# Optimization experiments

Hardware: AMD Instinct MI355X
Metric: run time of the kernel (lower is better)

## Reference

```python
import jax, jax.numpy as jnp
import numpy as np

N = 50000        # nodes
E = 800000       # directed edges (before self-loops)
F_IN = 128       # input node features
HID = 32         # hidden channels per head
HEADS = 4
NCLS = 8
EPS_BN = 1e-5
NEG_SLOPE = 0.2  # GATConv LeakyReLU default


def setup_inputs() -> dict:
    key = jax.random.key(0)
    ks = jax.random.split(key, 16)
    rn = lambda k, shape, s=0.1: jax.random.normal(k, shape, jnp.float32) * s
    inp = {}
    inp["x"] = jax.random.normal(ks[0], (N, F_IN), jnp.float32)
    inp["edge_index"] = jax.random.randint(ks[1], (2, E), 0, N, dtype=jnp.int32)
    # layer 0: F_IN -> HEADS*HID (concat)
    inp["W0"] = rn(ks[2], (F_IN, HEADS * HID))
    inp["as0"] = rn(ks[3], (HEADS, HID))
    inp["ad0"] = rn(ks[4], (HEADS, HID))
    inp["b0"] = jnp.zeros((HEADS * HID,), jnp.float32)
    inp["g0"] = jnp.ones((HEADS * HID,), jnp.float32)
    inp["bb0"] = jnp.zeros((HEADS * HID,), jnp.float32)
    inp["rm0"] = jnp.zeros((HEADS * HID,), jnp.float32)
    inp["rv0"] = jnp.ones((HEADS * HID,), jnp.float32)
    # layer 1: HEADS*HID -> HEADS*HID (concat)
    inp["W1"] = rn(ks[5], (HEADS * HID, HEADS * HID))
    inp["as1"] = rn(ks[6], (HEADS, HID))
    inp["ad1"] = rn(ks[7], (HEADS, HID))
    inp["b1"] = jnp.zeros((HEADS * HID,), jnp.float32)
    inp["g1"] = jnp.ones((HEADS * HID,), jnp.float32)
    inp["bb1"] = jnp.zeros((HEADS * HID,), jnp.float32)
    inp["rm1"] = jnp.zeros((HEADS * HID,), jnp.float32)
    inp["rv1"] = jnp.ones((HEADS * HID,), jnp.float32)
    # layer 2: HEADS*HID -> NCLS, heads=1, concat=False
    inp["W2"] = rn(ks[8], (HEADS * HID, NCLS))
    inp["as2"] = rn(ks[9], (1, NCLS))
    inp["ad2"] = rn(ks[10], (1, NCLS))
    inp["b2"] = jnp.zeros((NCLS,), jnp.float32)
    return inp


def gat_conv(x, src, dst, W, att_s, att_d, bias, H, C, concat):
    """PyG-style GATConv (eval mode, self-loops already appended to src/dst)."""
    n = x.shape[0]
    h = (x @ W).reshape(n, H, C)                       # [N,H,C]
    a_s = (h * att_s).sum(-1)                          # [N,H]
    a_d = (h * att_d).sum(-1)                          # [N,H]
    e = jax.nn.leaky_relu(a_s[src] + a_d[dst], NEG_SLOPE)  # [E,H]
    # numerically-stable segment softmax over incoming edges of each dst node
    m = jax.ops.segment_max(e, dst, num_segments=n)
    m = jnp.where(jnp.isfinite(m), m, 0.0)
    ex = jnp.exp(e - m[dst])
    den = jax.ops.segment_sum(ex, dst, num_segments=n)
    alpha = ex / (den[dst] + 1e-16)                    # [E,H]
    out = jax.ops.segment_sum(h[src] * alpha[:, :, None], dst, num_segments=n)  # [N,H,C]
    out = out.reshape(n, H * C) if concat else out.mean(axis=1)
    return out + bias


def bn_eval(x, g, b, rm, rv):
    return (x - rm) * jax.lax.rsqrt(rv + EPS_BN) * g + b


def reference(x, edge_index, W0, as0, ad0, b0, g0, bb0, rm0, rv0,
              W1, as1, ad1, b1, g1, bb1, rm1, rv1, W2, as2, ad2, b2):
    n = x.shape[0]
    loop = jnp.arange(n, dtype=edge_index.dtype)       # self-loops (PyG default)
    src = jnp.concatenate([edge_index[0], loop])
    dst = jnp.concatenate([edge_index[1], loop])
    h = gat_conv(x, src, dst, W0, as0, ad0, b0, HEADS, HID, True)
    h = jax.nn.elu(bn_eval(h, g0, bb0, rm0, rv0))
    h = gat_conv(h, src, dst, W1, as1, ad1, b1, HEADS, HID, True)
    h = jax.nn.elu(bn_eval(h, g1, bb1, rm1, rv1))
    h = gat_conv(h, src, dst, W2, as2, ad2, b2, 1, NCLS, False)
    return jax.nn.log_softmax(h, axis=1)
```

## Files before the change

kernel.cpp:

```cpp
#include <hip/hip_runtime.h>
#include <hip/hip_cooperative_groups.h>
#include <math.h>

namespace cg = cooperative_groups;

#define N_NODES 50000
#define N_EDGES 800000
#define ET (N_EDGES + N_NODES)
#define NEG 0.2f
#define EPS_BN 1e-5f

#define BSH 8
#define NBUCK ((N_NODES + 255) >> BSH)
#define EPB 4096
#define PB ((ET + EPB - 1) / EPB)
#define CAST_B 3125
#define PACK_B 64
#define GB ((N_NODES + 63) / 64)
#define AGG_U 12500
#define G2B ((N_NODES + 255) / 256)
#define PREP_U (PB + CAST_B + 2 * PACK_B)

typedef __attribute__((ext_vector_type(8))) short short8;
typedef __attribute__((ext_vector_type(4))) float f32x4;

__device__ __forceinline__ float lrelu(float e) { return e > 0.f ? e : NEG * e; }
__device__ __forceinline__ float bflo(unsigned u) { return __uint_as_float(u << 16); }
__device__ __forceinline__ float bfhi(unsigned u) { return __uint_as_float(u & 0xffff0000u); }
__device__ __forceinline__ unsigned f2bf(float f) {
    unsigned b = __float_as_uint(f);
    return (b + 0x7fffu + ((b >> 16) & 1u)) >> 16;
}

struct GatParams {
    const int* ei;
    const float* x;
    const float *W0, *as0, *ad0, *b0, *g0, *bb0, *rm0, *rv0;
    const float *W1, *as1, *ad1, *b1, *g1, *bb1, *rm1, *rv1;
    const float *W2, *as2, *ad2, *b2;
    float* out;
    unsigned short *xb, *Hb, *Xb, *W0p, *W1p;
    int *offs, *boffs, *bcur, *ssrc, *hists;
    int2* pairs;
    float *asn, *adn, *h2;
};


__device__ __forceinline__ void prep_unit(char* smem, int u, int tid,
        const int* __restrict__ ei, int* __restrict__ hists,
        const float* __restrict__ x, unsigned short* __restrict__ xb,
        const float* __restrict__ W0, unsigned short* __restrict__ W0p,
        const float* __restrict__ W1, unsigned short* __restrict__ W1p) {
    if (u < PB) {
        unsigned* h = (unsigned*)smem;
        __syncthreads();
        for (int i = tid; i < NBUCK; i += 256) h[i] = 0;
        __syncthreads();
        int e0 = u * EPB;
        #pragma unroll
        for (int k = 0; k < EPB / 256; k++) {
            int e = e0 + k * 256 + tid;
            if (e < ET) {
                int d = (e < N_EDGES) ? ei[N_EDGES + e] : (e - N_EDGES);
                atomicAdd(&h[d >> BSH], 1u);
            }
        }
        __syncthreads();
        for (int i = tid; i < NBUCK; i += 256)
            hists[u * NBUCK + i] = (int)h[i];
    } else if (u < PB + CAST_B) {
        int i = (u - PB) * 256 + tid;
        const float4* px = (const float4*)x + (size_t)i * 2;
        float4 a = px[0], c = px[1];
        uint4 o;
        o.x = f2bf(a.x) | (f2bf(a.y) << 16);
        o.y = f2bf(a.z) | (f2bf(a.w) << 16);
        o.z = f2bf(c.x) | (f2bf(c.y) << 16);
        o.w = f2bf(c.z) | (f2bf(c.w) << 16);
        ((uint4*)xb)[i] = o;
    } else {
        int pb = u - PB - CAST_B;
        const float* W = (pb < PACK_B) ? W0 : W1;
        unsigned short* Wp = (pb < PACK_B) ? W0p : W1p;
        int o = (pb & (PACK_B - 1)) * 256 + tid;
        int j = o & 7, lane = (o >> 3) & 63, kc = (o >> 9) & 3, t = o >> 11;
        int k = kc * 32 + ((lane >> 4) << 3) + j;
        int n = t * 16 + (lane & 15);
        Wp[o] = (unsigned short)f2bf(W[k * 128 + n]);
    }
}

__device__ __forceinline__ void scan_unit(char* smem, int tid,
        const int* __restrict__ hists, int* __restrict__ boffs,
        int* __restrict__ bcur, int* __restrict__ offs) {
    int* s = (int*)smem;
    int v = 0;
    if (tid < NBUCK) {
        const int* hp = hists + tid;
        #pragma unroll 8
        for (int uu = 0; uu < PB; uu++) v += hp[uu * NBUCK];
    }
    s[tid] = v;
    __syncthreads();
    for (int off = 1; off < 256; off <<= 1) {
        int x = (tid >= off) ? s[tid - off] : 0;
        __syncthreads();
        s[tid] += x;
        __syncthreads();
    }
    int excl = s[tid] - v;
    if (tid < NBUCK) { boffs[tid] = excl; bcur[tid] = excl; }
    if (tid == 0) { boffs[NBUCK] = ET; offs[N_NODES] = ET; }
    __syncthreads();
}

__device__ __forceinline__ void partition_unit(char* smem, int u, int tid,
        const int* __restrict__ ei, int* __restrict__ bcur, int2* __restrict__ pairs) {
    unsigned* hist = (unsigned*)smem;
    unsigned* base = hist + NBUCK;
    __syncthreads();
    for (int i = tid; i < NBUCK; i += 256) hist[i] = 0;
    __syncthreads();
    int e0 = u * EPB;
    #pragma unroll
    for (int k = 0; k < EPB / 256; k++) {
        int e = e0 + k * 256 + tid;
        if (e < ET) {
            int d = (e < N_EDGES) ? ei[N_EDGES + e] : (e - N_EDGES);
            atomicAdd(&hist[d >> BSH], 1u);
        }
    }
    __syncthreads();
    for (int i = tid; i < NBUCK; i += 256) {
        unsigned hh = hist[i];
        base[i] = hh ? (unsigned)atomicAdd(&bcur[i], (int)hh) : 0u;
        hist[i] = 0;
    }
    __syncthreads();
    #pragma unroll
    for (int k = 0; k < EPB / 256; k++) {
        int e = e0 + k * 256 + tid;
        if (e < ET) {
            int s, d;
            if (e < N_EDGES) { s = ei[e]; d = ei[N_EDGES + e]; }
            else             { s = d = e - N_EDGES; }
            int b = d >> BSH;
            unsigned lpos = atomicAdd(&hist[b], 1u);
            pairs[base[b] + lpos] = make_int2(s, d);
        }
    }
}

__device__ __forceinline__ void group_unit(char* smem, int u, int tid,
        const int2* __restrict__ pairs, const int* __restrict__ boffs,
        int* __restrict__ offs, int* __restrict__ ssrc) {
    int* cnt = (int*)smem;
    int* pfx = cnt + 256;
    __syncthreads();
    int n0 = u << BSH;
    int base = boffs[u], end = boffs[u + 1];
    cnt[tid] = 0;
    __syncthreads();
    for (int i = base + tid; i < end; i += 256)
        atomicAdd(&cnt[pairs[i].y & 255], 1);
    __syncthreads();
    int v = cnt[tid];
    pfx[tid] = v;
    __syncthreads();
    for (int off = 1; off < 256; off <<= 1) {
        int x = (tid >= off) ? pfx[tid - off] : 0;
        __syncthreads();
        pfx[tid] += x;
        __syncthreads();
    }
    int excl = pfx[tid] - v;
    if (n0 + tid < N_NODES) offs[n0 + tid] = base + excl;
    cnt[tid] = excl;
    __syncthreads();
    for (int i = base + tid; i < end; i += 256) {
        int2 pr = pairs[i];
        int pos = atomicAdd(&cnt[pr.y & 255], 1);
        ssrc[base + pos] = pr.x;
    }
}

__device__ __forceinline__ void gemm_phase(char* smem, int blk, int nblk,
        const unsigned short* __restrict__ Ab, const unsigned short* __restrict__ Wp,
        const float* __restrict__ att_s, const float* __restrict__ att_d,
        unsigned short* __restrict__ Hb, float* __restrict__ asn, float* __restrict__ adn) {
    float* tiles = (float*)smem;
    int tid = threadIdx.x;
    int wv = tid >> 6, lane = tid & 63;
    for (int u = blk; u < GB; u += nblk) {
        int base = u * 64;
        int mrow = base + wv * 16 + (lane & 15);
        if (mrow >= N_NODES) mrow = N_NODES - 1;
        int koff = (lane >> 4) * 8;

        f32x4 acc[8];
        #pragma unroll
        for (int t = 0; t < 8; t++) acc[t] = (f32x4){0.f, 0.f, 0.f, 0.f};
        #pragma unroll
        for (int kc = 0; kc < 4; kc++) {
            short8 a = *(const short8*)(Ab + (size_t)mrow * 128 + kc * 32 + koff);
            #pragma unroll
            for (int t = 0; t < 8; t++) {
                short8 b = *(const short8*)(Wp + (((t * 4 + kc) * 64 + lane) << 3));
                acc[t] = __builtin_amdgcn_mfma_f32_16x16x32_bf16(a, b, acc[t], 0, 0, 0);
            }
        }
        __syncthreads();
        int rbase = wv * 16 + (lane >> 4) * 4;
        int col = lane & 15;
        #pragma unroll
        for (int t = 0; t < 8; t++)
            #pragma unroll
            for (int r = 0; r < 4; r++)
                tiles[(rbase + r) * 132 + t * 16 + col] = acc[t][r];
        __syncthreads();

        #pragma unroll
        for (int it = 0; it < 4; it++) {
            int uu = tid + it * 256;
            int rl = uu >> 4, cg4 = uu & 15;
            int row = base + rl;
            if (row < N_NODES) {
                const float* pt = tiles + rl * 132 + cg4 * 8;
                float4 v0 = *(const float4*)(pt);
                float4 v1 = *(const float4*)(pt + 4);
                uint4 o;
                o.x = f2bf(v0.x) | (f2bf(v0.y) << 16);
                o.y = f2bf(v0.z) | (f2bf(v0.w) << 16);
                o.z = f2bf(v1.x) | (f2bf(v1.y) << 16);
                o.w = f2bf(v1.z) | (f2bf(v1.w) << 16);
                *(uint4*)(Hb + (size_t)row * 128 + cg4 * 8) = o;
            }
        }
        {
            int rl = tid >> 2, hd = tid & 3;
            int row = base + rl;
            if (row < N_NODES) {
                const float* hrow = tiles + rl * 132 + hd * 32;
                const float* as = att_s + hd * 32;
                const float* ad = att_d + hd * 32;
                float ps = 0.f, pd = 0.f;
                #pragma unroll
                for (int i = 0; i < 8; i++) {
                    float4 hv = *(const float4*)(hrow + i * 4);
                    float4 sv = *(const float4*)(as + i * 4);
                    float4 dv = *(const float4*)(ad + i * 4);
                    ps += hv.x * sv.x + hv.y * sv.y + hv.z * sv.z + hv.w * sv.w;
                    pd += hv.x * dv.x + hv.y * dv.y + hv.z * dv.z + hv.w * dv.w;
                }
                asn[row * 4 + hd] = ps;
                adn[row * 4 + hd] = pd;
            }
        }
        __syncthreads();
    }
}

__device__ __forceinline__ void aggregate_phase(char* smem, int blk, int nblk,
        const unsigned short* __restrict__ hb, const float* __restrict__ asn,
        const float* __restrict__ adn, const int* __restrict__ offs,
        const int* __restrict__ ssrc, const float* __restrict__ bias,
        const float* __restrict__ gamma, const float* __restrict__ beta,
        const float* __restrict__ rmean, const float* __restrict__ rvar,
        unsigned short* __restrict__ outb) {
    int2* sP = (int2*)smem;
    int tid = threadIdx.x;
    int wv = tid >> 6, lane = tid & 63;
    int half = lane >> 5, cl = lane & 31, hsel = cl >> 3;
    const char* hbase = (const char*)hb + cl * 8;
    int2* st0 = sP + (wv * 4 + 0) * 72;
    int2* st1 = sP + (wv * 4 + 1) * 72;
    int2* st2 = sP + (wv * 4 + 2) * 72;
    int2* st3 = sP + (wv * 4 + 3) * 72;
    const int2* pp = sP + (wv * 4 + hsel) * 72;

    for (int u = blk; u < AGG_U; u += nblk) {
        int node = u * 4 + wv;
        int beg = offs[node], deg = offs[node + 1] - beg;
        float4 ad4 = *(const float4*)(adn + node * 4);
        float a0 = 0.f, a1 = 0.f, a2 = 0.f, a3 = 0.f, denl = 0.f;

        for (int base0 = 0; base0 < deg; base0 += 64) {
            int j = base0 + lane;
            int soff = 0;
            float4 w4v = make_float4(0.f, 0.f, 0.f, 0.f);
            if (j < deg) {
                int s = ssrc[beg + j];
                soff = s << 8;
                float4 a = *(const float4*)(asn + s * 4);
                w4v.x = __expf(lrelu(a.x + ad4.x));
                w4v.y = __expf(lrelu(a.y + ad4.y));
                w4v.z = __expf(lrelu(a.z + ad4.z));
                w4v.w = __expf(lrelu(a.w + ad4.w));
            }
            st0[lane] = make_int2(soff, __float_as_int(w4v.x));
            st1[lane] = make_int2(soff, __float_as_int(w4v.y));
            st2[lane] = make_int2(soff, __float_as_int(w4v.z));
            st3[lane] = make_int2(soff, __float_as_int(w4v.w));
            int cnt = deg - base0; if (cnt > 64) cnt = 64;
            int bound = (cnt + 15) & ~15;
            for (int i = 0; i < bound; i += 16) {
                int2 p0 = pp[i + 0 + half],  p1 = pp[i + 2 + half];
                int2 p2 = pp[i + 4 + half],  p3 = pp[i + 6 + half];
                int2 p4 = pp[i + 8 + half],  p5 = pp[i + 10 + half];
                int2 p6 = pp[i + 12 + half], p7 = pp[i + 14 + half];
                uint2 u0 = *(const uint2*)(hbase + (unsigned)p0.x);
                uint2 u1 = *(const uint2*)(hbase + (unsigned)p1.x);
                uint2 u2 = *(const uint2*)(hbase + (unsigned)p2.x);
                uint2 u3 = *(const uint2*)(hbase + (unsigned)p3.x);
                uint2 u4 = *(const uint2*)(hbase + (unsigned)p4.x);
                uint2 u5 = *(const uint2*)(hbase + (unsigned)p5.x);
                uint2 u6 = *(const uint2*)(hbase + (unsigned)p6.x);
                uint2 u7 = *(const uint2*)(hbase + (unsigned)p7.x);
                float w0 = __int_as_float(p0.y), w1 = __int_as_float(p1.y);
                float w2 = __int_as_float(p2.y), w3 = __int_as_float(p3.y);
                float w4 = __int_as_float(p4.y), w5 = __int_as_float(p5.y);
                float w6 = __int_as_float(p6.y), w7 = __int_as_float(p7.y);
                denl += w0 + w1 + w2 + w3 + w4 + w5 + w6 + w7;
                a0 += w0 * bflo(u0.x); a1 += w0 * bfhi(u0.x); a2 += w0 * bflo(u0.y); a3 += w0 * bfhi(u0.y);
                a0 += w1 * bflo(u1.x); a1 += w1 * bfhi(u1.x); a2 += w1 * bflo(u1.y); a3 += w1 * bfhi(u1.y);
                a0 += w2 * bflo(u2.x); a1 += w2 * bfhi(u2.x); a2 += w2 * bflo(u2.y); a3 += w2 * bfhi(u2.y);
                a0 += w3 * bflo(u3.x); a1 += w3 * bfhi(u3.x); a2 += w3 * bflo(u3.y); a3 += w3 * bfhi(u3.y);
                a0 += w4 * bflo(u4.x); a1 += w4 * bfhi(u4.x); a2 += w4 * bflo(u4.y); a3 += w4 * bfhi(u4.y);
                a0 += w5 * bflo(u5.x); a1 += w5 * bfhi(u5.x); a2 += w5 * bflo(u5.y); a3 += w5 * bfhi(u5.y);
                a0 += w6 * bflo(u6.x); a1 += w6 * bfhi(u6.x); a2 += w6 * bflo(u6.y); a3 += w6 * bfhi(u6.y);
                a0 += w7 * bflo(u7.x); a1 += w7 * bfhi(u7.x); a2 += w7 * bflo(u7.y); a3 += w7 * bfhi(u7.y);
            }
        }
        a0 += __shfl_xor(a0, 32); a1 += __shfl_xor(a1, 32);
        a2 += __shfl_xor(a2, 32); a3 += __shfl_xor(a3, 32);
        denl += __shfl_xor(denl, 32);
        if (half == 0) {
            float inv = 1.f / (denl + 1e-16f);
            int c0 = cl * 4;
            float4 bi = *(const float4*)(bias + c0);
            float4 gm = *(const float4*)(gamma + c0);
            float4 bt = *(const float4*)(beta + c0);
            float4 rm = *(const float4*)(rmean + c0);
            float4 rv = *(const float4*)(rvar + c0);
            float o0 = a0 * inv + bi.x, o1 = a1 * inv + bi.y;
            float o2 = a2 * inv + bi.z, o3 = a3 * inv + bi.w;
            o0 = (o0 - rm.x) * rsqrtf(rv.x + EPS_BN) * gm.x + bt.x;
            o1 = (o1 - rm.y) * rsqrtf(rv.y + EPS_BN) * gm.y + bt.y;
            o2 = (o2 - rm.z) * rsqrtf(rv.z + EPS_BN) * gm.z + bt.z;
            o3 = (o3 - rm.w) * rsqrtf(rv.w + EPS_BN) * gm.w + bt.w;
            o0 = (o0 > 0.f) ? o0 : expm1f(o0);
            o1 = (o1 > 0.f) ? o1 : expm1f(o1);
            o2 = (o2 > 0.f) ? o2 : expm1f(o2);
            o3 = (o3 > 0.f) ? o3 : expm1f(o3);
            uint2 ob;
            ob.x = f2bf(o0) | (f2bf(o1) << 16);
            ob.y = f2bf(o2) | (f2bf(o3) << 16);
            *(uint2*)(outb + (size_t)node * 128 + c0) = ob;
        }
    }
}

__device__ __forceinline__ void gemm2_unit(char* smem, int u, int tid,
        const unsigned short* __restrict__ xb, const float* __restrict__ W2,
        const float* __restrict__ as2, const float* __restrict__ ad2,
        float* __restrict__ h2, float* __restrict__ asn, float* __restrict__ adn,
        bool loadW) {
    float* sW = (float*)smem;
    float* sas = sW + 1024;
    float* sad = sas + 8;
    if (loadW) {
        for (int i = tid; i < 1024; i += 256) sW[i] = W2[i];
        if (tid < 8) { sas[tid] = as2[tid]; sad[tid] = ad2[tid]; }
        __syncthreads();
    }
    int node = u * 256 + tid;
    if (node >= N_NODES) return;
    const uint4* xr = (const uint4*)(xb + (size_t)node * 128);
    float acc[8];
    #pragma unroll
    for (int c = 0; c < 8; c++) acc[c] = 0.f;
    for (int k8 = 0; k8 < 16; k8++) {
        uint4 uu = xr[k8];
        float f[8] = { bflo(uu.x), bfhi(uu.x), bflo(uu.y), bfhi(uu.y),
                       bflo(uu.z), bfhi(uu.z), bflo(uu.w), bfhi(uu.w) };
        int kb = k8 * 8;
        #pragma unroll
        for (int q = 0; q < 8; q++)
            #pragma unroll
            for (int c = 0; c < 8; c++)
                acc[c] += f[q] * sW[(kb + q) * 8 + c];
    }
    float ps = 0.f, pd = 0.f;
    #pragma unroll
    for (int c = 0; c < 8; c++) {
        h2[(size_t)node * 8 + c] = acc[c];
        ps += acc[c] * sas[c];
        pd += acc[c] * sad[c];
    }
    asn[node] = ps;
    adn[node] = pd;
}

__device__ __forceinline__ void agg2_unit(char* smem, int u, int tid,
        const float* __restrict__ h2, const float* __restrict__ asn,
        const float* __restrict__ adn, const int* __restrict__ offs,
        const int* __restrict__ ssrc, const float* __restrict__ b2,
        float* __restrict__ out) {
    int2* sP = (int2*)smem;
    int wv = tid >> 6, lane = tid & 63;
    int g = lane >> 3, c = lane & 7;
    int node = u * 4 + wv;
    int beg = offs[node], end = offs[node + 1];
    int deg = end - beg;
    float adv = adn[node];
    float den = 0.f, acc = 0.f;
    int2* ws = sP + wv * 64;
    for (int base = 0; base < deg; base += 64) {
        int j = base + lane;
        int s = 0; float w = 0.f;
        if (j < deg) {
            s = ssrc[beg + j];
            w = __expf(lrelu(asn[s] + adv));
            den += w;
        }
        ws[lane] = make_int2(s, __float_as_int(w));
        int cnt = deg - base; if (cnt > 64) cnt = 64;
        int nIt = (cnt + 15) >> 4;
        for (int i = 0; i < nIt; i++) {
            int e = i * 16 + g;
            int2 p0 = ws[e];
            int2 p1 = ws[e + 8];
            acc += __int_as_float(p0.y) * h2[(((unsigned)p0.x) << 3) + c];
            acc += __int_as_float(p1.y) * h2[(((unsigned)p1.x) << 3) + c];
        }
    }
    acc += __shfl_xor(acc, 8); acc += __shfl_xor(acc, 16); acc += __shfl_xor(acc, 32);
    #pragma unroll
    for (int off = 32; off; off >>= 1) den += __shfl_xor(den, off);
    float o = acc / (den + 1e-16f) + b2[c];
    float mx = o;
    mx = fmaxf(mx, __shfl_xor(mx, 1));
    mx = fmaxf(mx, __shfl_xor(mx, 2));
    mx = fmaxf(mx, __shfl_xor(mx, 4));
    float ex = __expf(o - mx);
    float sm = ex;
    sm += __shfl_xor(sm, 1); sm += __shfl_xor(sm, 2); sm += __shfl_xor(sm, 4);
    if (g == 0) out[(size_t)node * 8 + c] = o - mx - logf(sm);
}


__global__ __launch_bounds__(256, 3) void gat_mega(GatParams p) {
    cg::grid_group grid = cg::this_grid();
    __shared__ __align__(16) char smem[64 * 132 * 4];
    const int blk = blockIdx.x, nblk = gridDim.x, tid = threadIdx.x;

    for (int u = blk; u < PREP_U; u += nblk)
        prep_unit(smem, u, tid, p.ei, p.hists, p.x, p.xb, p.W0, p.W0p, p.W1, p.W1p);
    grid.sync();

    if (blk == 0) scan_unit(smem, tid, p.hists, p.boffs, p.bcur, p.offs);
    gemm_phase(smem, blk, nblk, p.xb, p.W0p, p.as0, p.ad0, p.Hb, p.asn, p.adn);
    grid.sync();

    for (int u = blk; u < PB; u += nblk)
        partition_unit(smem, u, tid, p.ei, p.bcur, p.pairs);
    grid.sync();

    for (int u = blk; u < NBUCK; u += nblk)
        group_unit(smem, u, tid, p.pairs, p.boffs, p.offs, p.ssrc);
    grid.sync();

    aggregate_phase(smem, blk, nblk, p.Hb, p.asn, p.adn, p.offs, p.ssrc,
                    p.b0, p.g0, p.bb0, p.rm0, p.rv0, p.Xb);
    grid.sync();

    gemm_phase(smem, blk, nblk, p.Xb, p.W1p, p.as1, p.ad1, p.Hb, p.asn, p.adn);
    grid.sync();

    aggregate_phase(smem, blk, nblk, p.Hb, p.asn, p.adn, p.offs, p.ssrc,
                    p.b1, p.g1, p.bb1, p.rm1, p.rv1, p.Xb);
    grid.sync();

    {
        float* sW = (float*)smem;
        float* sas = sW + 1024;
        float* sad = sas + 8;
        __syncthreads();
        for (int i = tid; i < 1024; i += 256) sW[i] = p.W2[i];
        if (tid < 8) { sas[tid] = p.as2[tid]; sad[tid] = p.ad2[tid]; }
        __syncthreads();
        for (int u = blk; u < G2B; u += nblk)
            gemm2_unit(smem, u, tid, p.Xb, p.W2, p.as2, p.ad2, p.h2, p.asn, p.adn, false);
    }
    grid.sync();

    for (int u = blk; u < AGG_U; u += nblk) {
        __syncthreads();
        agg2_unit(smem, u, tid, p.h2, p.asn, p.adn, p.offs, p.ssrc, p.b2, p.out);
    }
}


__global__ __launch_bounds__(256) void k_prep(GatParams p) {
    __shared__ __align__(16) char smem[1024];
    prep_unit(smem, blockIdx.x, threadIdx.x, p.ei, p.hists, p.x, p.xb,
              p.W0, p.W0p, p.W1, p.W1p);
}
__global__ __launch_bounds__(256) void k_scan(GatParams p) {
    __shared__ __align__(16) char smem[1024];
    scan_unit(smem, threadIdx.x, p.hists, p.boffs, p.bcur, p.offs);
}
__global__ __launch_bounds__(256) void k_partition(GatParams p) {
    __shared__ __align__(16) char smem[2048];
    partition_unit(smem, blockIdx.x, threadIdx.x, p.ei, p.bcur, p.pairs);
}
__global__ __launch_bounds__(256) void k_group(GatParams p) {
    __shared__ __align__(16) char smem[2048];
    group_unit(smem, blockIdx.x, threadIdx.x, p.pairs, p.boffs, p.offs, p.ssrc);
}
__global__ __launch_bounds__(256) void k_gemm(GatParams p, int layer) {
    __shared__ __align__(16) char smem[64 * 132 * 4];
    if (layer == 0)
        gemm_phase(smem, blockIdx.x, gridDim.x, p.xb, p.W0p, p.as0, p.ad0,
                   p.Hb, p.asn, p.adn);
    else
        gemm_phase(smem, blockIdx.x, gridDim.x, p.Xb, p.W1p, p.as1, p.ad1,
                   p.Hb, p.asn, p.adn);
}
__global__ __launch_bounds__(256) void k_agg(GatParams p, int layer) {
    __shared__ __align__(16) char smem[4 * 4 * 72 * 8];
    if (layer == 0)
        aggregate_phase(smem, blockIdx.x, gridDim.x, p.Hb, p.asn, p.adn, p.offs,
                        p.ssrc, p.b0, p.g0, p.bb0, p.rm0, p.rv0, p.Xb);
    else
        aggregate_phase(smem, blockIdx.x, gridDim.x, p.Hb, p.asn, p.adn, p.offs,
                        p.ssrc, p.b1, p.g1, p.bb1, p.rm1, p.rv1, p.Xb);
}
__global__ __launch_bounds__(256) void k_gemm2(GatParams p) {
    __shared__ __align__(16) char smem[1040 * 4];
    gemm2_unit(smem, blockIdx.x, threadIdx.x, p.Xb, p.W2, p.as2, p.ad2,
               p.h2, p.asn, p.adn, true);
}
__global__ __launch_bounds__(256) void k_agg2(GatParams p) {
    __shared__ __align__(16) char smem[4 * 64 * 8];
    agg2_unit(smem, blockIdx.x, threadIdx.x, p.h2, p.asn, p.adn, p.offs,
              p.ssrc, p.b2, p.out);
}


extern "C" void kernel_launch(void* const* d_in, const int* in_sizes, int n_in,
                              void* d_out, int out_size, void* d_ws, size_t ws_size,
                              hipStream_t stream) {
    GatParams prm;
    prm.ei  = (const int*)d_in[1];
    prm.x   = (const float*)d_in[0];
    prm.W0  = (const float*)d_in[2];
    prm.as0 = (const float*)d_in[3];  prm.ad0 = (const float*)d_in[4];
    prm.b0  = (const float*)d_in[5];  prm.g0  = (const float*)d_in[6];
    prm.bb0 = (const float*)d_in[7];  prm.rm0 = (const float*)d_in[8];
    prm.rv0 = (const float*)d_in[9];
    prm.W1  = (const float*)d_in[10];
    prm.as1 = (const float*)d_in[11]; prm.ad1 = (const float*)d_in[12];
    prm.b1  = (const float*)d_in[13]; prm.g1  = (const float*)d_in[14];
    prm.bb1 = (const float*)d_in[15]; prm.rm1 = (const float*)d_in[16];
    prm.rv1 = (const float*)d_in[17];
    prm.W2  = (const float*)d_in[18];
    prm.as2 = (const float*)d_in[19]; prm.ad2 = (const float*)d_in[20];
    prm.b2  = (const float*)d_in[21];
    prm.out = (float*)d_out;

    char* w = (char*)d_ws;
    size_t off = 0;
    auto carve = [&](size_t bytes) {
        void* p = w + off;
        off += (bytes + 255) & ~(size_t)255;
        return p;
    };
    prm.xb    = (unsigned short*)carve((size_t)N_NODES * 128 * 2);
    prm.Hb    = (unsigned short*)carve((size_t)N_NODES * 128 * 2);
    prm.Xb    = (unsigned short*)carve((size_t)N_NODES * 128 * 2);
    prm.W0p   = (unsigned short*)carve(16384 * 2);
    prm.W1p   = (unsigned short*)carve(16384 * 2);
    prm.offs  = (int*)carve((size_t)(N_NODES + 1) * 4);
    prm.boffs = (int*)carve((size_t)(NBUCK + 1) * 4);
    prm.bcur  = (int*)carve((size_t)NBUCK * 4);
    prm.ssrc  = (int*)carve((size_t)ET * 4);
    prm.hists = (int*)carve((size_t)PB * NBUCK * 4);
    prm.pairs = (int2*)carve((size_t)ET * 8);
    prm.asn   = (float*)carve((size_t)N_NODES * 4 * 4);
    prm.adn   = (float*)carve((size_t)N_NODES * 4 * 4);
    prm.h2    = (float*)carve((size_t)N_NODES * 8 * 4);
    (void)ws_size; (void)in_sizes; (void)n_in; (void)out_size;

    bool coop_done = false;
    int mb = 0;
    if (hipOccupancyMaxActiveBlocksPerMultiprocessor(
            &mb, (const void*)gat_mega, 256, 0) == hipSuccess && mb >= 2) {
        int nb = (mb >= 3) ? 768 : 512;
        void* args[] = { (void*)&prm };
        if (hipLaunchCooperativeKernel((const void*)gat_mega, dim3(nb), dim3(256),
                                       args, 0, stream) == hipSuccess)
            coop_done = true;
    }
    if (!coop_done) {
        k_prep<<<PREP_U, 256, 0, stream>>>(prm);
        k_scan<<<1, 256, 0, stream>>>(prm);
        k_partition<<<PB, 256, 0, stream>>>(prm);
        k_group<<<NBUCK, 256, 0, stream>>>(prm);
        k_gemm<<<GB, 256, 0, stream>>>(prm, 0);
        k_agg<<<AGG_U, 256, 0, stream>>>(prm, 0);
        k_gemm<<<GB, 256, 0, stream>>>(prm, 1);
        k_agg<<<AGG_U, 256, 0, stream>>>(prm, 1);
        k_gemm2<<<G2B, 256, 0, stream>>>(prm);
        k_agg2<<<AGG_U, 256, 0, stream>>>(prm);
    }
}
```

Baseline: 328.0 us.

## Replace cooperative megakernel with sequence of separate kernel launches

Measured after the change: 291.5 us. 11.1% less time.

```diff
diff --git a/kernel.cpp b/kernel.cpp
--- a/kernel.cpp
+++ b/kernel.cpp
@@ -1,8 +1,5 @@
 #include <hip/hip_runtime.h>
-#include <hip/hip_cooperative_groups.h>
 #include <math.h>
-
-namespace cg = cooperative_groups;
 
 #define N_NODES 50000
 #define N_EDGES 800000
@@ -46,14 +43,10 @@
 };
 
 
-__device__ __forceinline__ void prep_unit(char* smem, int u, int tid,
-        const int* __restrict__ ei, int* __restrict__ hists,
-        const float* __restrict__ x, unsigned short* __restrict__ xb,
-        const float* __restrict__ W0, unsigned short* __restrict__ W0p,
-        const float* __restrict__ W1, unsigned short* __restrict__ W1p) {
+__global__ __launch_bounds__(256) void k_prep(GatParams p) {
+    __shared__ unsigned h[NBUCK];
+    int u = blockIdx.x, tid = threadIdx.x;
     if (u < PB) {
-        unsigned* h = (unsigned*)smem;
-        __syncthreads();
         for (int i = tid; i < NBUCK; i += 256) h[i] = 0;
         __syncthreads();
         int e0 = u * EPB;
@@ -61,27 +54,27 @@
         for (int k = 0; k < EPB / 256; k++) {
             int e = e0 + k * 256 + tid;
             if (e < ET) {
-                int d = (e < N_EDGES) ? ei[N_EDGES + e] : (e - N_EDGES);
+                int d = (e < N_EDGES) ? p.ei[N_EDGES + e] : (e - N_EDGES);
                 atomicAdd(&h[d >> BSH], 1u);
             }
         }
         __syncthreads();
         for (int i = tid; i < NBUCK; i += 256)
-            hists[u * NBUCK + i] = (int)h[i];
+            p.hists[u * NBUCK + i] = (int)h[i];
     } else if (u < PB + CAST_B) {
         int i = (u - PB) * 256 + tid;
-        const float4* px = (const float4*)x + (size_t)i * 2;
+        const float4* px = (const float4*)p.x + (size_t)i * 2;
         float4 a = px[0], c = px[1];
         uint4 o;
         o.x = f2bf(a.x) | (f2bf(a.y) << 16);
         o.y = f2bf(a.z) | (f2bf(a.w) << 16);
         o.z = f2bf(c.x) | (f2bf(c.y) << 16);
         o.w = f2bf(c.z) | (f2bf(c.w) << 16);
-        ((uint4*)xb)[i] = o;
+        ((uint4*)p.xb)[i] = o;
     } else {
         int pb = u - PB - CAST_B;
-        const float* W = (pb < PACK_B) ? W0 : W1;
-        unsigned short* Wp = (pb < PACK_B) ? W0p : W1p;
+        const float* W = (pb < PACK_B) ? p.W0 : p.W1;
+        unsigned short* Wp = (pb < PACK_B) ? p.W0p : p.W1p;
         int o = (pb & (PACK_B - 1)) * 256 + tid;
         int j = o & 7, lane = (o >> 3) & 63, kc = (o >> 9) & 3, t = o >> 11;
         int k = kc * 32 + ((lane >> 4) << 3) + j;
@@ -90,13 +83,12 @@
     }
 }
 
-__device__ __forceinline__ void scan_unit(char* smem, int tid,
-        const int* __restrict__ hists, int* __restrict__ boffs,
-        int* __restrict__ bcur, int* __restrict__ offs) {
-    int* s = (int*)smem;
+__global__ __launch_bounds__(256) void k_scan(GatParams p) {
+    __shared__ int s[256];
+    int tid = threadIdx.x;
     int v = 0;
     if (tid < NBUCK) {
-        const int* hp = hists + tid;
+        const int* hp = p.hists + tid;
         #pragma unroll 8
         for (int uu = 0; uu < PB; uu++) v += hp[uu * NBUCK];
     }
@@ -109,31 +101,29 @@
         __syncthreads();
     }
     int excl = s[tid] - v;
-    if (tid < NBUCK) { boffs[tid] = excl; bcur[tid] = excl; }
-    if (tid == 0) { boffs[NBUCK] = ET; offs[N_NODES] = ET; }
-    __syncthreads();
-}
-
-__device__ __forceinline__ void partition_unit(char* smem, int u, int tid,
-        const int* __restrict__ ei, int* __restrict__ bcur, int2* __restrict__ pairs) {
-    unsigned* hist = (unsigned*)smem;
-    unsigned* base = hist + NBUCK;
-    __syncthreads();
+    if (tid < NBUCK) { p.boffs[tid] = excl; p.bcur[tid] = excl; }
+    if (tid == 0) { p.boffs[NBUCK] = ET; p.offs[N_NODES] = ET; }
+}
+
+__global__ __launch_bounds__(256) void k_partition(GatParams p) {
+    __shared__ unsigned hist[NBUCK];
+    __shared__ unsigned base[NBUCK];
+    int tid = threadIdx.x;
+    int e0 = blockIdx.x * EPB;
     for (int i = tid; i < NBUCK; i += 256) hist[i] = 0;
     __syncthreads();
-    int e0 = u * EPB;
     #pragma unroll
     for (int k = 0; k < EPB / 256; k++) {
         int e = e0 + k * 256 + tid;
         if (e < ET) {
-            int d = (e < N_EDGES) ? ei[N_EDGES + e] : (e - N_EDGES);
+            int d = (e < N_EDGES) ? p.ei[N_EDGES + e] : (e - N_EDGES);
             atomicAdd(&hist[d >> BSH], 1u);
         }
     }
     __syncthreads();
     for (int i = tid; i < NBUCK; i += 256) {
         unsigned hh = hist[i];
-        base[i] = hh ? (unsigned)atomicAdd(&bcur[i], (int)hh) : 0u;
+        base[i] = hh ? (unsigned)atomicAdd(&p.bcur[i], (int)hh) : 0u;
         hist[i] = 0;
     }
     __syncthreads();
@@ -142,27 +132,25 @@
         int e = e0 + k * 256 + tid;
         if (e < ET) {
             int s, d;
-            if (e < N_EDGES) { s = ei[e]; d = ei[N_EDGES + e]; }
+            if (e < N_EDGES) { s = p.ei[e]; d = p.ei[N_EDGES + e]; }
             else             { s = d = e - N_EDGES; }
             int b = d >> BSH;
             unsigned lpos = atomicAdd(&hist[b], 1u);
-            pairs[base[b] + lpos] = make_int2(s, d);
-        }
-    }
-}
-
-__device__ __forceinline__ void group_unit(char* smem, int u, int tid,
-        const int2* __restrict__ pairs, const int* __restrict__ boffs,
-        int* __restrict__ offs, int* __restrict__ ssrc) {
-    int* cnt = (int*)smem;
-    int* pfx = cnt + 256;
-    __syncthreads();
+            p.pairs[base[b] + lpos] = make_int2(s, d);
+        }
+    }
+}
+
+__global__ __launch_bounds__(256) void k_group(GatParams p) {
+    __shared__ int cnt[256];
+    __shared__ int pfx[256];
+    int u = blockIdx.x, tid = threadIdx.x;
     int n0 = u << BSH;
-    int base = boffs[u], end = boffs[u + 1];
+    int base = p.boffs[u], end = p.boffs[u + 1];
     cnt[tid] = 0;
     __syncthreads();
     for (int i = base + tid; i < end; i += 256)
-        atomicAdd(&cnt[pairs[i].y & 255], 1);
+        atomicAdd(&cnt[p.pairs[i].y & 255], 1);
     __syncthreads();
     int v = cnt[tid];
     pfx[tid] = v;
@@ -174,208 +162,209 @@
         __syncthreads();
     }
     int excl = pfx[tid] - v;
-    if (n0 + tid < N_NODES) offs[n0 + tid] = base + excl;
+    if (n0 + tid < N_NODES) p.offs[n0 + tid] = base + excl;
     cnt[tid] = excl;
     __syncthreads();
     for (int i = base + tid; i < end; i += 256) {
-        int2 pr = pairs[i];
+        int2 pr = p.pairs[i];
         int pos = atomicAdd(&cnt[pr.y & 255], 1);
-        ssrc[base + pos] = pr.x;
-    }
-}
-
-__device__ __forceinline__ void gemm_phase(char* smem, int blk, int nblk,
-        const unsigned short* __restrict__ Ab, const unsigned short* __restrict__ Wp,
-        const float* __restrict__ att_s, const float* __restrict__ att_d,
-        unsigned short* __restrict__ Hb, float* __restrict__ asn, float* __restrict__ adn) {
-    float* tiles = (float*)smem;
+        p.ssrc[base + pos] = pr.x;
+    }
+}
+
+
+__global__ __launch_bounds__(256) void k_gemm(GatParams p, int layer) {
+    __shared__ float tiles[64 * 132];
+    const unsigned short* Ab = (layer == 0) ? p.xb : p.Xb;
+    const unsigned short* Wp = (layer == 0) ? p.W0p : p.W1p;
+    const float* att_s = (layer == 0) ? p.as0 : p.as1;
+    const float* att_d = (layer == 0) ? p.ad0 : p.ad1;
     int tid = threadIdx.x;
     int wv = tid >> 6, lane = tid & 63;
-    for (int u = blk; u < GB; u += nblk) {
-        int base = u * 64;
-        int mrow = base + wv * 16 + (lane & 15);
-        if (mrow >= N_NODES) mrow = N_NODES - 1;
-        int koff = (lane >> 4) * 8;
-
-        f32x4 acc[8];
+    int base = blockIdx.x * 64;
+    int mrow = base + wv * 16 + (lane & 15);
+    if (mrow >= N_NODES) mrow = N_NODES - 1;
+    int koff = (lane >> 4) * 8;
+
+    f32x4 acc[8];
+    #pragma unroll
+    for (int t = 0; t < 8; t++) acc[t] = (f32x4){0.f, 0.f, 0.f, 0.f};
+    #pragma unroll
+    for (int kc = 0; kc < 4; kc++) {
+        short8 a = *(const short8*)(Ab + (size_t)mrow * 128 + kc * 32 + koff);
         #pragma unroll
-        for (int t = 0; t < 8; t++) acc[t] = (f32x4){0.f, 0.f, 0.f, 0.f};
+        for (int t = 0; t < 8; t++) {
+            short8 b = *(const short8*)(Wp + (((t * 4 + kc) * 64 + lane) << 3));
+            acc[t] = __builtin_amdgcn_mfma_f32_16x16x32_bf16(a, b, acc[t], 0, 0, 0);
+        }
+    }
+    int rbase = wv * 16 + (lane >> 4) * 4;
+    int col = lane & 15;
+    #pragma unroll
+    for (int t = 0; t < 8; t++)
         #pragma unroll
-        for (int kc = 0; kc < 4; kc++) {
-            short8 a = *(const short8*)(Ab + (size_t)mrow * 128 + kc * 32 + koff);
+        for (int r = 0; r < 4; r++)
+            tiles[(rbase + r) * 132 + t * 16 + col] = acc[t][r];
+    __syncthreads();
+
+    #pragma unroll
+    for (int it = 0; it < 4; it++) {
+        int uu = tid + it * 256;
+        int rl = uu >> 4, cg4 = uu & 15;
+        int row = base + rl;
+        if (row < N_NODES) {
+            const float* pt = tiles + rl * 132 + cg4 * 8;
+            float4 v0 = *(const float4*)(pt);
+            float4 v1 = *(const float4*)(pt + 4);
+            uint4 o;
+            o.x = f2bf(v0.x) | (f2bf(v0.y) << 16);
+            o.y = f2bf(v0.z) | (f2bf(v0.w) << 16);
+            o.z = f2bf(v1.x) | (f2bf(v1.y) << 16);
+            o.w = f2bf(v1.z) | (f2bf(v1.w) << 16);
+            *(uint4*)(p.Hb + (size_t)row * 128 + cg4 * 8) = o;
+        }
+    }
+    {
+        int rl = tid >> 2, hd = tid & 3;
+        int row = base + rl;
+        if (row < N_NODES) {
+            const float* hrow = tiles + rl * 132 + hd * 32;
+            const float* as = att_s + hd * 32;
+            const float* ad = att_d + hd * 32;
+            float ps = 0.f, pd = 0.f;
             #pragma unroll
-            for (int t = 0; t < 8; t++) {
-                short8 b = *(const short8*)(Wp + (((t * 4 + kc) * 64 + lane) << 3));
-                acc[t] = __builtin_amdgcn_mfma_f32_16x16x32_bf16(a, b, acc[t], 0, 0, 0);
+            for (int i = 0; i < 8; i++) {
+                float4 hv = *(const float4*)(hrow + i * 4);
+                float4 sv = *(const float4*)(as + i * 4);
+                float4 dv = *(const float4*)(ad + i * 4);
+                ps += hv.x * sv.x + hv.y * sv.y + hv.z * sv.z + hv.w * sv.w;
+                pd += hv.x * dv.x + hv.y * dv.y + hv.z * dv.z + hv.w * dv.w;
             }
-        }
-        __syncthreads();
-        int rbase = wv * 16 + (lane >> 4) * 4;
-        int col = lane & 15;
-        #pragma unroll
-        for (int t = 0; t < 8; t++)
-            #pragma unroll
-            for (int r = 0; r < 4; r++)
-                tiles[(rbase + r) * 132 + t * 16 + col] = acc[t][r];
-        __syncthreads();
-
-        #pragma unroll
-        for (int it = 0; it < 4; it++) {
-            int uu = tid + it * 256;
-            int rl = uu >> 4, cg4 = uu & 15;
-            int row = base + rl;
-            if (row < N_NODES) {
-                const float* pt = tiles + rl * 132 + cg4 * 8;
-                float4 v0 = *(const float4*)(pt);
-                float4 v1 = *(const float4*)(pt + 4);
-                uint4 o;
-                o.x = f2bf(v0.x) | (f2bf(v0.y) << 16);
-                o.y = f2bf(v0.z) | (f2bf(v0.w) << 16);
-                o.z = f2bf(v1.x) | (f2bf(v1.y) << 16);
-                o.w = f2bf(v1.z) | (f2bf(v1.w) << 16);
-                *(uint4*)(Hb + (size_t)row * 128 + cg4 * 8) = o;
-            }
-        }
-        {
-            int rl = tid >> 2, hd = tid & 3;
-            int row = base + rl;
-            if (row < N_NODES) {
-                const float* hrow = tiles + rl * 132 + hd * 32;
-                const float* as = att_s + hd * 32;
-                const float* ad = att_d + hd * 32;
-                float ps = 0.f, pd = 0.f;
-                #pragma unroll
-                for (int i = 0; i < 8; i++) {
-                    float4 hv = *(const float4*)(hrow + i * 4);
-                    float4 sv = *(const float4*)(as + i * 4);
-                    float4 dv = *(const float4*)(ad + i * 4);
-                    ps += hv.x * sv.x + hv.y * sv.y + hv.z * sv.z + hv.w * sv.w;
-                    pd += hv.x * dv.x + hv.y * dv.y + hv.z * dv.z + hv.w * dv.w;
-                }
-                asn[row * 4 + hd] = ps;
-                adn[row * 4 + hd] = pd;
-            }
-        }
-        __syncthreads();
-    }
-}
-
-__device__ __forceinline__ void aggregate_phase(char* smem, int blk, int nblk,
-        const unsigned short* __restrict__ hb, const float* __restrict__ asn,
-        const float* __restrict__ adn, const int* __restrict__ offs,
-        const int* __restrict__ ssrc, const float* __restrict__ bias,
-        const float* __restrict__ gamma, const float* __restrict__ beta,
-        const float* __restrict__ rmean, const float* __restrict__ rvar,
-        unsigned short* __restrict__ outb) {
-    int2* sP = (int2*)smem;
+            p.asn[row * 4 + hd] = ps;
+            p.adn[row * 4 + hd] = pd;
+        }
+    }
+}
+
+
+__global__ __launch_bounds__(256) void k_agg(GatParams p, int layer) {
+    __shared__ int2 sP[4 * 4 * 72];
+    const float* bias  = (layer == 0) ? p.b0  : p.b1;
+    const float* gamma = (layer == 0) ? p.g0  : p.g1;
+    const float* beta  = (layer == 0) ? p.bb0 : p.bb1;
+    const float* rmean = (layer == 0) ? p.rm0 : p.rm1;
+    const float* rvar  = (layer == 0) ? p.rv0 : p.rv1;
     int tid = threadIdx.x;
     int wv = tid >> 6, lane = tid & 63;
     int half = lane >> 5, cl = lane & 31, hsel = cl >> 3;
-    const char* hbase = (const char*)hb + cl * 8;
+    const char* hbase = (const char*)p.Hb + cl * 8;
     int2* st0 = sP + (wv * 4 + 0) * 72;
     int2* st1 = sP + (wv * 4 + 1) * 72;
     int2* st2 = sP + (wv * 4 + 2) * 72;
     int2* st3 = sP + (wv * 4 + 3) * 72;
     const int2* pp = sP + (wv * 4 + hsel) * 72;
 
-    for (int u = blk; u < AGG_U; u += nblk) {
-        int node = u * 4 + wv;
-        int beg = offs[node], deg = offs[node + 1] - beg;
-        float4 ad4 = *(const float4*)(adn + node * 4);
-        float a0 = 0.f, a1 = 0.f, a2 = 0.f, a3 = 0.f, denl = 0.f;
-
-        for (int base0 = 0; base0 < deg; base0 += 64) {
-            int j = base0 + lane;
-            int soff = 0;
-            float4 w4v = make_float4(0.f, 0.f, 0.f, 0.f);
-            if (j < deg) {
-                int s = ssrc[beg + j];
-                soff = s << 8;
-                float4 a = *(const float4*)(asn + s * 4);
-                w4v.x = __expf(lrelu(a.x + ad4.x));
-                w4v.y = __expf(lrelu(a.y + ad4.y));
-                w4v.z = __expf(lrelu(a.z + ad4.z));
-                w4v.w = __expf(lrelu(a.w + ad4.w));
-            }
-            st0[lane] = make_int2(soff, __float_as_int(w4v.x));
-            st1[lane] = make_int2(soff, __float_as_int(w4v.y));
-            st2[lane] = make_int2(soff, __float_as_int(w4v.z));
-            st3[lane] = make_int2(soff, __float_as_int(w4v.w));
-            int cnt = deg - base0; if (cnt > 64) cnt = 64;
-            int bound = (cnt + 15) & ~15;
-            for (int i = 0; i < bound; i += 16) {
-                int2 p0 = pp[i + 0 + half],  p1 = pp[i + 2 + half];
-                int2 p2 = pp[i + 4 + half],  p3 = pp[i + 6 + half];
-                int2 p4 = pp[i + 8 + half],  p5 = pp[i + 10 + half];
-                int2 p6 = pp[i + 12 + half], p7 = pp[i + 14 + half];
-                uint2 u0 = *(const uint2*)(hbase + (unsigned)p0.x);
-                uint2 u1 = *(const uint2*)(hbase + (unsigned)p1.x);
-                uint2 u2 = *(const uint2*)(hbase + (unsigned)p2.x);
-                uint2 u3 = *(const uint2*)(hbase + (unsigned)p3.x);
-                uint2 u4 = *(const uint2*)(hbase + (unsigned)p4.x);
-                uint2 u5 = *(const uint2*)(hbase + (unsigned)p5.x);
-                uint2 u6 = *(const uint2*)(hbase + (unsigned)p6.x);
-                uint2 u7 = *(const uint2*)(hbase + (unsigned)p7.x);
-                float w0 = __int_as_float(p0.y), w1 = __int_as_float(p1.y);
-                float w2 = __int_as_float(p2.y), w3 = __int_as_float(p3.y);
-                float w4 = __int_as_float(p4.y), w5 = __int_as_float(p5.y);
-                float w6 = __int_as_float(p6.y), w7 = __int_as_float(p7.y);
-                denl += w0 + w1 + w2 + w3 + w4 + w5 + w6 + w7;
-                a0 += w0 * bflo(u0.x); a1 += w0 * bfhi(u0.x); a2 += w0 * bflo(u0.y); a3 += w0 * bfhi(u0.y);
-                a0 += w1 * bflo(u1.x); a1 += w1 * bfhi(u1.x); a2 += w1 * bflo(u1.y); a3 += w1 * bfhi(u1.y);
-                a0 += w2 * bflo(u2.x); a1 += w2 * bfhi(u2.x); a2 += w2 * bflo(u2.y); a3 += w2 * bfhi(u2.y);
-                a0 += w3 * bflo(u3.x); a1 += w3 * bfhi(u3.x); a2 += w3 * bflo(u3.y); a3 += w3 * bfhi(u3.y);
-                a0 += w4 * bflo(u4.x); a1 += w4 * bfhi(u4.x); a2 += w4 * bflo(u4.y); a3 += w4 * bfhi(u4.y);
-                a0 += w5 * bflo(u5.x); a1 += w5 * bfhi(u5.x); a2 += w5 * bflo(u5.y); a3 += w5 * bfhi(u5.y);
-                a0 += w6 * bflo(u6.x); a1 += w6 * bfhi(u6.x); a2 += w6 * bflo(u6.y); a3 += w6 * bfhi(u6.y);
-                a0 += w7 * bflo(u7.x); a1 += w7 * bfhi(u7.x); a2 += w7 * bflo(u7.y); a3 += w7 * bfhi(u7.y);
-            }
-        }
-        a0 += __shfl_xor(a0, 32); a1 += __shfl_xor(a1, 32);
-        a2 += __shfl_xor(a2, 32); a3 += __shfl_xor(a3, 32);
-        denl += __shfl_xor(denl, 32);
-        if (half == 0) {
-            float inv = 1.f / (denl + 1e-16f);
-            int c0 = cl * 4;
-            float4 bi = *(const float4*)(bias + c0);
-            float4 gm = *(const float4*)(gamma + c0);
-            float4 bt = *(const float4*)(beta + c0);
-            float4 rm = *(const float4*)(rmean + c0);
-            float4 rv = *(const float4*)(rvar + c0);
-            float o0 = a0 * inv + bi.x, o1 = a1 * inv + bi.y;
-            float o2 = a2 * inv + bi.z, o3 = a3 * inv + bi.w;
-            o0 = (o0 - rm.x) * rsqrtf(rv.x + EPS_BN) * gm.x + bt.x;
-            o1 = (o1 - rm.y) * rsqrtf(rv.y + EPS_BN) * gm.y + bt.y;
-            o2 = (o2 - rm.z) * rsqrtf(rv.z + EPS_BN) * gm.z + bt.z;
-            o3 = (o3 - rm.w) * rsqrtf(rv.w + EPS_BN) * gm.w + bt.w;
-            o0 = (o0 > 0.f) ? o0 : expm1f(o0);
-            o1 = (o1 > 0.f) ? o1 : expm1f(o1);
-            o2 = (o2 > 0.f) ? o2 : expm1f(o2);
-            o3 = (o3 > 0.f) ? o3 : expm1f(o3);
-            uint2 ob;
-            ob.x = f2bf(o0) | (f2bf(o1) << 16);
-            ob.y = f2bf(o2) | (f2bf(o3) << 16);
-            *(uint2*)(outb + (size_t)node * 128 + c0) = ob;
-        }
-    }
-}
-
-__device__ __forceinline__ void gemm2_unit(char* smem, int u, int tid,
-        const unsigned short* __restrict__ xb, const float* __restrict__ W2,
-        const float* __restrict__ as2, const float* __restrict__ ad2,
-        float* __restrict__ h2, float* __restrict__ asn, float* __restrict__ adn,
-        bool loadW) {
-    float* sW = (float*)smem;
-    float* sas = sW + 1024;
-    float* sad = sas + 8;
-    if (loadW) {
-        for (int i = tid; i < 1024; i += 256) sW[i] = W2[i];
-        if (tid < 8) { sas[tid] = as2[tid]; sad[tid] = ad2[tid]; }
-        __syncthreads();
-    }
-    int node = u * 256 + tid;
+    int node = blockIdx.x * 4 + wv;
+    int beg = p.offs[node], deg = p.offs[node + 1] - beg;
+    float4 ad4 = *(const float4*)(p.adn + node * 4);
+    float a0 = 0.f, a1 = 0.f, a2 = 0.f, a3 = 0.f, denl = 0.f;
+
+    for (int base0 = 0; base0 < deg; base0 += 64) {
+        int j = base0 + lane;
+        int soff = 0;
+        float4 w4v = make_float4(0.f, 0.f, 0.f, 0.f);
+        if (j < deg) {
+            int s = p.ssrc[beg + j];
+            soff = s << 8;
+            float4 a = *(const float4*)(p.asn + s * 4);
+            w4v.x = __expf(lrelu(a.x + ad4.x));
+            w4v.y = __expf(lrelu(a.y + ad4.y));
+            w4v.z = __expf(lrelu(a.z + ad4.z));
+            w4v.w = __expf(lrelu(a.w + ad4.w));
+        }
+        st0[lane] = make_int2(soff, __float_as_int(w4v.x));
+        st1[lane] = make_int2(soff, __float_as_int(w4v.y));
+        st2[lane] = make_int2(soff, __float_as_int(w4v.z));
+        st3[lane] = make_int2(soff, __float_as_int(w4v.w));
+        int cnt = deg - base0; if (cnt > 64) cnt = 64;
+
+        int i = 0;
+        for (; i + 16 <= cnt; i += 16) {
+            int2 p0 = pp[i + 0 + half],  p1 = pp[i + 2 + half];
+            int2 p2 = pp[i + 4 + half],  p3 = pp[i + 6 + half];
+            int2 p4 = pp[i + 8 + half],  p5 = pp[i + 10 + half];
+            int2 p6 = pp[i + 12 + half], p7 = pp[i + 14 + half];
+            uint2 u0 = *(const uint2*)(hbase + (unsigned)p0.x);
+            uint2 u1 = *(const uint2*)(hbase + (unsigned)p1.x);
+            uint2 u2 = *(const uint2*)(hbase + (unsigned)p2.x);
+            uint2 u3 = *(const uint2*)(hbase + (unsigned)p3.x);
+            uint2 u4 = *(const uint2*)(hbase + (unsigned)p4.x);
+            uint2 u5 = *(const uint2*)(hbase + (unsigned)p5.x);
+            uint2 u6 = *(const uint2*)(hbase + (unsigned)p6.x);
+            uint2 u7 = *(const uint2*)(hbase + (unsigned)p7.x);
+            float w0 = __int_as_float(p0.y), w1 = __int_as_float(p1.y);
+            float w2 = __int_as_float(p2.y), w3 = __int_as_float(p3.y);
+            float w4 = __int_as_float(p4.y), w5 = __int_as_float(p5.y);
+            float w6 = __int_as_float(p6.y), w7 = __int_as_float(p7.y);
+            denl += w0 + w1 + w2 + w3 + w4 + w5 + w6 + w7;
+            a0 += w0 * bflo(u0.x); a1 += w0 * bfhi(u0.x); a2 += w0 * bflo(u0.y); a3 += w0 * bfhi(u0.y);
+            a0 += w1 * bflo(u1.x); a1 += w1 * bfhi(u1.x); a2 += w1 * bflo(u1.y); a3 += w1 * bfhi(u1.y);
+            a0 += w2 * bflo(u2.x); a1 += w2 * bfhi(u2.x); a2 += w2 * bflo(u2.y); a3 += w2 * bfhi(u2.y);
+            a0 += w3 * bflo(u3.x); a1 += w3 * bfhi(u3.x); a2 += w3 * bflo(u3.y); a3 += w3 * bfhi(u3.y);
+            a0 += w4 * bflo(u4.x); a1 += w4 * bfhi(u4.x); a2 += w4 * bflo(u4.y); a3 += w4 * bfhi(u4.y);
+            a0 += w5 * bflo(u5.x); a1 += w5 * bfhi(u5.x); a2 += w5 * bflo(u5.y); a3 += w5 * bfhi(u5.y);
+            a0 += w6 * bflo(u6.x); a1 += w6 * bfhi(u6.x); a2 += w6 * bflo(u6.y); a3 += w6 * bfhi(u6.y);
+            a0 += w7 * bflo(u7.x); a1 += w7 * bfhi(u7.x); a2 += w7 * bflo(u7.y); a3 += w7 * bfhi(u7.y);
+        }
+        for (; i < cnt; i += 4) {
+            int2 p0 = pp[i + half], p1 = pp[i + 2 + half];
+            uint2 u0 = *(const uint2*)(hbase + (unsigned)p0.x);
+            uint2 u1 = *(const uint2*)(hbase + (unsigned)p1.x);
+            float w0 = __int_as_float(p0.y), w1 = __int_as_float(p1.y);
+            denl += w0 + w1;
+            a0 += w0 * bflo(u0.x); a1 += w0 * bfhi(u0.x); a2 += w0 * bflo(u0.y); a3 += w0 * bfhi(u0.y);
+            a0 += w1 * bflo(u1.x); a1 += w1 * bfhi(u1.x); a2 += w1 * bflo(u1.y); a3 += w1 * bfhi(u1.y);
+        }
+    }
+    a0 += __shfl_xor(a0, 32); a1 += __shfl_xor(a1, 32);
+    a2 += __shfl_xor(a2, 32); a3 += __shfl_xor(a3, 32);
+    denl += __shfl_xor(denl, 32);
+    if (half == 0) {
+        float inv = 1.f / (denl + 1e-16f);
+        int c0 = cl * 4;
+        float4 bi = *(const float4*)(bias + c0);
+        float4 gm = *(const float4*)(gamma + c0);
+        float4 bt = *(const float4*)(beta + c0);
+        float4 rm = *(const float4*)(rmean + c0);
+        float4 rv = *(const float4*)(rvar + c0);
+        float o0 = a0 * inv + bi.x, o1 = a1 * inv + bi.y;
+        float o2 = a2 * inv + bi.z, o3 = a3 * inv + bi.w;
+        o0 = (o0 - rm.x) * rsqrtf(rv.x + EPS_BN) * gm.x + bt.x;
+        o1 = (o1 - rm.y) * rsqrtf(rv.y + EPS_BN) * gm.y + bt.y;
+        o2 = (o2 - rm.z) * rsqrtf(rv.z + EPS_BN) * gm.z + bt.z;
+        o3 = (o3 - rm.w) * rsqrtf(rv.w + EPS_BN) * gm.w + bt.w;
+        o0 = (o0 > 0.f) ? o0 : expm1f(o0);
+        o1 = (o1 > 0.f) ? o1 : expm1f(o1);
+        o2 = (o2 > 0.f) ? o2 : expm1f(o2);
+        o3 = (o3 > 0.f) ? o3 : expm1f(o3);
+        uint2 ob;
+        ob.x = f2bf(o0) | (f2bf(o1) << 16);
+        ob.y = f2bf(o2) | (f2bf(o3) << 16);
+        *(uint2*)(p.Xb + (size_t)node * 128 + c0) = ob;
+    }
+}
+
+
+__global__ __launch_bounds__(256) void k_gemm2(GatParams p) {
+    __shared__ float sW[128 * 8];
+    __shared__ float sas[8], sad[8];
+    int tid = threadIdx.x;
+    for (int i = tid; i < 1024; i += 256) sW[i] = p.W2[i];
+    if (tid < 8) { sas[tid] = p.as2[tid]; sad[tid] = p.ad2[tid]; }
+    __syncthreads();
+    int node = blockIdx.x * 256 + tid;
     if (node >= N_NODES) return;
-    const uint4* xr = (const uint4*)(xb + (size_t)node * 128);
+    const uint4* xr = (const uint4*)(p.Xb + (size_t)node * 128);
     float acc[8];
     #pragma unroll
     for (int c = 0; c < 8; c++) acc[c] = 0.f;
@@ -393,51 +382,52 @@
     float ps = 0.f, pd = 0.f;
     #pragma unroll
     for (int c = 0; c < 8; c++) {
-        h2[(size_t)node * 8 + c] = acc[c];
+        p.h2[(size_t)node * 8 + c] = acc[c];
         ps += acc[c] * sas[c];
         pd += acc[c] * sad[c];
     }
-    asn[node] = ps;
-    adn[node] = pd;
-}
-
-__device__ __forceinline__ void agg2_unit(char* smem, int u, int tid,
-        const float* __restrict__ h2, const float* __restrict__ asn,
-        const float* __restrict__ adn, const int* __restrict__ offs,
-        const int* __restrict__ ssrc, const float* __restrict__ b2,
-        float* __restrict__ out) {
-    int2* sP = (int2*)smem;
+    p.asn[node] = ps;
+    p.adn[node] = pd;
+}
+
+
+__global__ __launch_bounds__(256) void k_agg2(GatParams p) {
+    __shared__ int2 sP[4 * 64];
+    int tid = threadIdx.x;
     int wv = tid >> 6, lane = tid & 63;
     int g = lane >> 3, c = lane & 7;
-    int node = u * 4 + wv;
-    int beg = offs[node], end = offs[node + 1];
+    int node = blockIdx.x * 4 + wv;
+    int beg = p.offs[node], end = p.offs[node + 1];
     int deg = end - beg;
-    float adv = adn[node];
+    float adv = p.adn[node];
     float den = 0.f, acc = 0.f;
     int2* ws = sP + wv * 64;
     for (int base = 0; base < deg; base += 64) {
         int j = base + lane;
         int s = 0; float w = 0.f;
         if (j < deg) {
-            s = ssrc[beg + j];
-            w = __expf(lrelu(asn[s] + adv));
+            s = p.ssrc[beg + j];
+            w = __expf(lrelu(p.asn[s] + adv));
             den += w;
         }
         ws[lane] = make_int2(s, __float_as_int(w));
         int cnt = deg - base; if (cnt > 64) cnt = 64;
-        int nIt = (cnt + 15) >> 4;
-        for (int i = 0; i < nIt; i++) {
-            int e = i * 16 + g;
-            int2 p0 = ws[e];
-            int2 p1 = ws[e + 8];
-            acc += __int_as_float(p0.y) * h2[(((unsigned)p0.x) << 3) + c];
-            acc += __int_as_float(p1.y) * h2[(((unsigned)p1.x) << 3) + c];
+        int i = 0;
+        for (; i + 16 <= cnt; i += 16) {
+            int2 p0 = ws[i + g];
+            int2 p1 = ws[i + 8 + g];
+            acc += __int_as_float(p0.y) * p.h2[(((unsigned)p0.x) << 3) + c];
+            acc += __int_as_float(p1.y) * p.h2[(((unsigned)p1.x) << 3) + c];
+        }
+        for (; i < cnt; i += 8) {
+            int2 p0 = ws[i + g];
+            acc += __int_as_float(p0.y) * p.h2[(((unsigned)p0.x) << 3) + c];
         }
     }
     acc += __shfl_xor(acc, 8); acc += __shfl_xor(acc, 16); acc += __shfl_xor(acc, 32);
     #pragma unroll
     for (int off = 32; off; off >>= 1) den += __shfl_xor(den, off);
-    float o = acc / (den + 1e-16f) + b2[c];
+    float o = acc / (den + 1e-16f) + p.b2[c];
     float mx = o;
     mx = fmaxf(mx, __shfl_xor(mx, 1));
     mx = fmaxf(mx, __shfl_xor(mx, 2));
@@ -445,106 +435,7 @@
     float ex = __expf(o - mx);
     float sm = ex;
     sm += __shfl_xor(sm, 1); sm += __shfl_xor(sm, 2); sm += __shfl_xor(sm, 4);
-    if (g == 0) out[(size_t)node * 8 + c] = o - mx - logf(sm);
-}
-
-
-__global__ __launch_bounds__(256, 3) void gat_mega(GatParams p) {
-    cg::grid_group grid = cg::this_grid();
-    __shared__ __align__(16) char smem[64 * 132 * 4];
-    const int blk = blockIdx.x, nblk = gridDim.x, tid = threadIdx.x;
-
-    for (int u = blk; u < PREP_U; u += nblk)
-        prep_unit(smem, u, tid, p.ei, p.hists, p.x, p.xb, p.W0, p.W0p, p.W1, p.W1p);
-    grid.sync();
-
-    if (blk == 0) scan_unit(smem, tid, p.hists, p.boffs, p.bcur, p.offs);
-    gemm_phase(smem, blk, nblk, p.xb, p.W0p, p.as0, p.ad0, p.Hb, p.asn, p.adn);
-    grid.sync();
-
-    for (int u = blk; u < PB; u += nblk)
-        partition_unit(smem, u, tid, p.ei, p.bcur, p.pairs);
-    grid.sync();
-
-    for (int u = blk; u < NBUCK; u += nblk)
-        group_unit(smem, u, tid, p.pairs, p.boffs, p.offs, p.ssrc);
-    grid.sync();
-
-    aggregate_phase(smem, blk, nblk, p.Hb, p.asn, p.adn, p.offs, p.ssrc,
-                    p.b0, p.g0, p.bb0, p.rm0, p.rv0, p.Xb);
-    grid.sync();
-
-    gemm_phase(smem, blk, nblk, p.Xb, p.W1p, p.as1, p.ad1, p.Hb, p.asn, p.adn);
-    grid.sync();
-
-    aggregate_phase(smem, blk, nblk, p.Hb, p.asn, p.adn, p.offs, p.ssrc,
-                    p.b1, p.g1, p.bb1, p.rm1, p.rv1, p.Xb);
-    grid.sync();
-
-    {
-        float* sW = (float*)smem;
-        float* sas = sW + 1024;
-        float* sad = sas + 8;
-        __syncthreads();
-        for (int i = tid; i < 1024; i += 256) sW[i] = p.W2[i];
-        if (tid < 8) { sas[tid] = p.as2[tid]; sad[tid] = p.ad2[tid]; }
-        __syncthreads();
-        for (int u = blk; u < G2B; u += nblk)
-            gemm2_unit(smem, u, tid, p.Xb, p.W2, p.as2, p.ad2, p.h2, p.asn, p.adn, false);
-    }
-    grid.sync();
-
-    for (int u = blk; u < AGG_U; u += nblk) {
-        __syncthreads();
-        agg2_unit(smem, u, tid, p.h2, p.asn, p.adn, p.offs, p.ssrc, p.b2, p.out);
-    }
-}
-
-
-__global__ __launch_bounds__(256) void k_prep(GatParams p) {
-    __shared__ __align__(16) char smem[1024];
-    prep_unit(smem, blockIdx.x, threadIdx.x, p.ei, p.hists, p.x, p.xb,
-              p.W0, p.W0p, p.W1, p.W1p);
-}
-__global__ __launch_bounds__(256) void k_scan(GatParams p) {
-    __shared__ __align__(16) char smem[1024];
-    scan_unit(smem, threadIdx.x, p.hists, p.boffs, p.bcur, p.offs);
-}
-__global__ __launch_bounds__(256) void k_partition(GatParams p) {
-    __shared__ __align__(16) char smem[2048];
-    partition_unit(smem, blockIdx.x, threadIdx.x, p.ei, p.bcur, p.pairs);
-}
-__global__ __launch_bounds__(256) void k_group(GatParams p) {
-    __shared__ __align__(16) char smem[2048];
-    group_unit(smem, blockIdx.x, threadIdx.x, p.pairs, p.boffs, p.offs, p.ssrc);
-}
-__global__ __launch_bounds__(256) void k_gemm(GatParams p, int layer) {
-    __shared__ __align__(16) char smem[64 * 132 * 4];
-    if (layer == 0)
-        gemm_phase(smem, blockIdx.x, gridDim.x, p.xb, p.W0p, p.as0, p.ad0,
-                   p.Hb, p.asn, p.adn);
-    else
-        gemm_phase(smem, blockIdx.x, gridDim.x, p.Xb, p.W1p, p.as1, p.ad1,
-                   p.Hb, p.asn, p.adn);
-}
-__global__ __launch_bounds__(256) void k_agg(GatParams p, int layer) {
-    __shared__ __align__(16) char smem[4 * 4 * 72 * 8];
-    if (layer == 0)
-        aggregate_phase(smem, blockIdx.x, gridDim.x, p.Hb, p.asn, p.adn, p.offs,
-                        p.ssrc, p.b0, p.g0, p.bb0, p.rm0, p.rv0, p.Xb);
-    else
-        aggregate_phase(smem, blockIdx.x, gridDim.x, p.Hb, p.asn, p.adn, p.offs,
-                        p.ssrc, p.b1, p.g1, p.bb1, p.rm1, p.rv1, p.Xb);
-}
-__global__ __launch_bounds__(256) void k_gemm2(GatParams p) {
-    __shared__ __align__(16) char smem[1040 * 4];
-    gemm2_unit(smem, blockIdx.x, threadIdx.x, p.Xb, p.W2, p.as2, p.ad2,
-               p.h2, p.asn, p.adn, true);
-}
-__global__ __launch_bounds__(256) void k_agg2(GatParams p) {
-    __shared__ __align__(16) char smem[4 * 64 * 8];
-    agg2_unit(smem, blockIdx.x, threadIdx.x, p.h2, p.asn, p.adn, p.offs,
-              p.ssrc, p.b2, p.out);
+    if (g == 0) p.out[(size_t)node * 8 + c] = o - mx - logf(sm);
 }
 
 
@@ -592,26 +483,14 @@
     prm.h2    = (float*)carve((size_t)N_NODES * 8 * 4);
     (void)ws_size; (void)in_sizes; (void)n_in; (void)out_size;
 
-    bool coop_done = false;
-    int mb = 0;
-    if (hipOccupancyMaxActiveBlocksPerMultiprocessor(
-            &mb, (const void*)gat_mega, 256, 0) == hipSuccess && mb >= 2) {
-        int nb = (mb >= 3) ? 768 : 512;
-        void* args[] = { (void*)&prm };
-        if (hipLaunchCooperativeKernel((const void*)gat_mega, dim3(nb), dim3(256),
-                                       args, 0, stream) == hipSuccess)
-            coop_done = true;
-    }
-    if (!coop_done) {
-        k_prep<<<PREP_U, 256, 0, stream>>>(prm);
-        k_scan<<<1, 256, 0, stream>>>(prm);
-        k_partition<<<PB, 256, 0, stream>>>(prm);
-        k_group<<<NBUCK, 256, 0, stream>>>(prm);
-        k_gemm<<<GB, 256, 0, stream>>>(prm, 0);
-        k_agg<<<AGG_U, 256, 0, stream>>>(prm, 0);
-        k_gemm<<<GB, 256, 0, stream>>>(prm, 1);
-        k_agg<<<AGG_U, 256, 0, stream>>>(prm, 1);
-        k_gemm2<<<G2B, 256, 0, stream>>>(prm);
-        k_agg2<<<AGG_U, 256, 0, stream>>>(prm);
-    }
-}
+    k_prep<<<PREP_U, 256, 0, stream>>>(prm);
+    k_scan<<<1, 256, 0, stream>>>(prm);
+    k_partition<<<PB, 256, 0, stream>>>(prm);
+    k_group<<<NBUCK, 256, 0, stream>>>(prm);
+    k_gemm<<<GB, 256, 0, stream>>>(prm, 0);
+    k_agg<<<AGG_U, 256, 0, stream>>>(prm, 0);
+    k_gemm<<<GB, 256, 0, stream>>>(prm, 1);
+    k_agg<<<AGG_U, 256, 0, stream>>>(prm, 1);
+    k_gemm2<<<G2B, 256, 0, stream>>>(prm);
+    k_agg2<<<AGG_U, 256, 0, stream>>>(prm);
+}
```
